# Kernel tuning notes

Hardware: AMD Instinct MI355X
Metric: run time of the kernel (lower is better)

Reference implementation:

```python
import jax, jax.numpy as jnp
import numpy as np

K = 3
STRIDE = 1
PADDING = 1
INVALID = -1.0


def _unfold(x, k, stride, padding, fill):
    # x: [B, C, H, W] -> patches [B, C, k, k, P] matching torch F.unfold ordering
    x = jnp.pad(x, ((0, 0), (0, 0), (padding, padding), (padding, padding)),
                constant_values=fill)
    # feature dim ordered channel-major (C, kh, kw), same as torch unfold
    p = jax.lax.conv_general_dilated_patches(x, (k, k), (stride, stride), 'VALID')
    b, _, ho, wo = p.shape
    c = x.shape[1]
    return p.reshape(b, c, k, k, ho * wo), ho, wo


def setup_inputs() -> dict:
    key = jax.random.key(0)
    k1, k2, k3, k4 = jax.random.split(key, 4)
    B, C, H, W = 8, 64, 128, 128
    OC = 64
    inp = jax.random.normal(k1, (B, C, H, W), dtype=jnp.float32)
    mask = jax.random.randint(k2, (B, H, W), 0, 4).astype(jnp.float32)
    conv = jax.random.normal(k3, (OC, C, K, K), dtype=jnp.float32) * 0.05
    bias = jax.random.normal(k4, (OC,), dtype=jnp.float32) * 0.05
    return {"inp": inp, "mask": mask, "conv": conv, "bias": bias}


def reference(inp, mask, conv, bias):
    k, stride, padding = K, STRIDE, PADDING
    b, c, h_in, w_in = inp.shape
    oc = conv.shape[0]
    center = (k - 1) // 2

    inp_patched, ho, wo = _unfold(inp, k, stride, padding, INVALID)       # [B,C,k,k,P]
    mask_patched, _, _ = _unfold(mask[:, None], k, stride, padding, INVALID)  # [B,1,k,k,P]
    mask_patched = mask_patched[:, 0]                                      # [B,k,k,P]

    center_val = mask_patched[:, center:center + 1, center:center + 1, :]  # [B,1,1,P]
    mask_eq = (mask_patched == center_val).astype(inp.dtype)               # [B,k,k,P]

    masked_input = inp_patched * mask_eq[:, None]                          # [B,C,k,k,P]
    m_norm = (k * k) / jnp.clip(mask_eq.reshape(b, k * k, -1).sum(axis=1), 1e-8)  # [B,P]

    masked_input = masked_input.reshape(b, c, k * k, -1)                   # [B,C,kk,P]
    w = conv.reshape(oc, c, k * k)                                         # [O,C,kk]
    out = jnp.einsum('bcxp,ocx->bop', masked_input, w)                     # [B,O,P]
    out = out * m_norm[:, None, :]
    out = out.reshape(b, oc, ho, wo)
    out = out + bias[None, :, None, None]

    mask_out = mask_patched[:, center, center, :].reshape(b, 1, ho, wo)
    return out, mask_out
```

## Files before the change

### kernel.cpp

```cpp
#include <hip/hip_runtime.h>
#include <stdint.h>

#define HW   128
#define CIN  64
#define OCN  64
#define NB   8

typedef __attribute__((ext_vector_type(8)))  short short8;
typedef __attribute__((ext_vector_type(16))) float floatx16;
typedef unsigned long long u64;

union F8 { short8 s; u64 u[2]; uint32_t d[4]; };

static __device__ __forceinline__ ushort f2bf(float f) {
    uint32_t u = __float_as_uint(f);
    uint32_t r = (u + 0x7FFFu + ((u >> 16) & 1u)) >> 16;
    return (ushort)r;
}

__global__ void wprep_kernel(const float* __restrict__ conv, ushort* __restrict__ wb) {
    int idx = blockIdx.x * 256 + threadIdx.x;
    int tap = idx >> 12;
    int r   = idx & 4095;
    int oc  = r >> 6;
    int c   = r & 63;
    wb[idx] = f2bf(conv[(oc * 64 + c) * 9 + tap]);
}

#define XS_CSTR 68
#define XS_ROW  (HW * XS_CSTR)
#define AS_STR  68
#define LDS_BYTES 80640

__global__ __launch_bounds__(256, 2)
void iconv_main(const float* __restrict__ inp, const float* __restrict__ mask,
                const ushort* __restrict__ wb, const float* __restrict__ bias,
                float* __restrict__ out)
{
    extern __shared__ char smem[];
    ushort* Xs = (ushort*)smem;
    ushort* As = Xs + 4 * XS_ROW;
    float*  Ms = (float*)(smem + 78336);
    float*  Bb = (float*)(smem + 78336 + 2048);

    const int tid  = threadIdx.x;
    const int bb   = blockIdx.x >> 6;
    const int y0   = (blockIdx.x & 63) << 1;
    const int lane = tid & 63;
    const int l31  = lane & 31;
    const int lh   = lane >> 5;
    const int w    = tid >> 6;
    const int yloc = w >> 1;
    const int xw   = (w & 1) * 64;
    const int y    = y0 + yloc;

    {
        const int cp = tid & 31;
        const int xq = (tid >> 5) * 16;
        const float* base0 = inp + ((size_t)(bb * CIN + 2 * cp) * HW) * HW;
        #pragma unroll
        for (int rr = 0; rr < 4; ++rr) {
            int gy = y0 - 1 + rr;
            if (gy >= 0 && gy < HW) {
                const float4* q0 = (const float4*)(base0 + (size_t)gy * HW + xq);
                const float4* q1 = (const float4*)(base0 + (size_t)HW * HW + (size_t)gy * HW + xq);
                float4 v0[4], v1[4];
                #pragma unroll
                for (int i = 0; i < 4; ++i) { v0[i] = q0[i]; v1[i] = q1[i]; }
                ushort* xrow = Xs + rr * XS_ROW + xq * XS_CSTR + 2 * cp;
                const float* f0 = (const float*)v0;
                const float* f1 = (const float*)v1;
                #pragma unroll
                for (int i = 0; i < 16; ++i) {
                    uint32_t p = (uint32_t)f2bf(f0[i]) | ((uint32_t)f2bf(f1[i]) << 16);
                    *(uint32_t*)(xrow + i * XS_CSTR) = p;
                }
            }
        }
    }
    {
        int rr = tid >> 6, x0 = (tid & 63) * 2;
        int gy = y0 - 1 + rr;
        if (gy >= 0 && gy < HW) {
            float2 v = *(const float2*)(mask + ((size_t)bb * HW + gy) * HW + x0);
            Ms[rr * HW + x0]     = v.x;
            Ms[rr * HW + x0 + 1] = v.y;
        }
    }
    if (tid < OCN) Bb[tid] = bias[tid];

    uint4 wv0 = *(const uint4*)(wb + tid * 16);
    uint4 wv1 = *(const uint4*)(wb + tid * 16 + 8);

    __syncthreads();

    uint32_t sel[9][2];
    float norm0, norm1;
    {
        int cnt0 = 0, cnt1 = 0;
        int xq0 = xw + l31, xq1 = xw + 32 + l31;
        float m00 = Ms[(1 + yloc) * HW + xq0];
        float m01 = Ms[(1 + yloc) * HW + xq1];
        #pragma unroll
        for (int t = 0; t < 9; ++t) {
            int dy = t / 3 - 1, dx = t % 3 - 1;
            int ny = y + dy;
            bool vy = (ny >= 0) && (ny < HW);
            int rbase = (1 + yloc + dy) * HW;
            {
                int nx = xq0 + dx;
                bool ok = vy && (nx >= 0) && (nx < HW);
                int nxc = nx < 0 ? 0 : (nx > HW - 1 ? HW - 1 : nx);
                bool eq = ok && (Ms[rbase + nxc] == m00);
                sel[t][0] = eq ? 0xFFFFFFFFu : 0u;
                cnt0 += eq ? 1 : 0;
            }
            {
                int nx = xq1 + dx;
                bool ok = vy && (nx >= 0) && (nx < HW);
                int nxc = nx < 0 ? 0 : (nx > HW - 1 ? HW - 1 : nx);
                bool eq = ok && (Ms[rbase + nxc] == m01);
                sel[t][1] = eq ? 0xFFFFFFFFu : 0u;
                cnt1 += eq ? 1 : 0;
            }
        }
        norm0 = 9.0f / (float)cnt0;
        norm1 = 9.0f / (float)cnt1;
    }

    floatx16 acc00 = {0,0,0,0,0,0,0,0,0,0,0,0,0,0,0,0};
    floatx16 acc01 = {0,0,0,0,0,0,0,0,0,0,0,0,0,0,0,0};
    floatx16 acc10 = {0,0,0,0,0,0,0,0,0,0,0,0,0,0,0,0};
    floatx16 acc11 = {0,0,0,0,0,0,0,0,0,0,0,0,0,0,0,0};

    const ushort* A0p = As + l31 * AS_STR + lh * 8;
    const ushort* A1p = As + (l31 + 32) * AS_STR + lh * 8;

    #pragma unroll
    for (int t = 0; t < 9; ++t) {
        if (t > 0) __syncthreads();
        {
            int oc = tid >> 2, c0 = (tid & 3) << 4;
            ushort* dst = As + oc * AS_STR + c0;
            *(uint2*)(dst)      = make_uint2(wv0.x, wv0.y);
            *(uint2*)(dst + 4)  = make_uint2(wv0.z, wv0.w);
            *(uint2*)(dst + 8)  = make_uint2(wv1.x, wv1.y);
            *(uint2*)(dst + 12) = make_uint2(wv1.z, wv1.w);
        }
        if (t < 8) {
            wv0 = *(const uint4*)(wb + (t + 1) * 4096 + tid * 16);
            wv1 = *(const uint4*)(wb + (t + 1) * 4096 + tid * 16 + 8);
        }
        __syncthreads();

        const int dy = t / 3 - 1, dx = t % 3 - 1;
        const int rrB = 1 + yloc + dy;
        int xa = xw + l31 + dx;
        int xb0c = xa < 0 ? 0 : (xa > HW - 1 ? HW - 1 : xa);
        int xa1 = xa + 32;
        int xb1c = xa1 < 0 ? 0 : (xa1 > HW - 1 ? HW - 1 : xa1);
        const ushort* B0p = Xs + rrB * XS_ROW + xb0c * XS_CSTR + lh * 8;
        const ushort* B1p = Xs + rrB * XS_ROW + xb1c * XS_CSTR + lh * 8;
        const uint32_t s0 = sel[t][0], s1 = sel[t][1];

        #pragma unroll
        for (int ks = 0; ks < 4; ++ks) {
            F8 a0, a1, b0, b1;
            a0.u[0] = *(const u64*)(A0p + ks * 16);
            a0.u[1] = *(const u64*)(A0p + ks * 16 + 4);
            a1.u[0] = *(const u64*)(A1p + ks * 16);
            a1.u[1] = *(const u64*)(A1p + ks * 16 + 4);
            b0.u[0] = *(const u64*)(B0p + ks * 16);
            b0.u[1] = *(const u64*)(B0p + ks * 16 + 4);
            b1.u[0] = *(const u64*)(B1p + ks * 16);
            b1.u[1] = *(const u64*)(B1p + ks * 16 + 4);
            b0.d[0] &= s0; b0.d[1] &= s0; b0.d[2] &= s0; b0.d[3] &= s0;
            b1.d[0] &= s1; b1.d[1] &= s1; b1.d[2] &= s1; b1.d[3] &= s1;
            acc00 = __builtin_amdgcn_mfma_f32_32x32x16_bf16(a0.s, b0.s, acc00, 0, 0, 0);
            acc01 = __builtin_amdgcn_mfma_f32_32x32x16_bf16(a0.s, b1.s, acc01, 0, 0, 0);
            acc10 = __builtin_amdgcn_mfma_f32_32x32x16_bf16(a1.s, b0.s, acc10, 0, 0, 0);
            acc11 = __builtin_amdgcn_mfma_f32_32x32x16_bf16(a1.s, b1.s, acc11, 0, 0, 0);
        }
    }

    float* outp = out + (size_t)bb * OCN * HW * HW + (size_t)y * HW;
    #pragma unroll
    for (int mt = 0; mt < 2; ++mt) {
        #pragma unroll
        for (int nt = 0; nt < 2; ++nt) {
            floatx16 a = (mt == 0) ? (nt == 0 ? acc00 : acc01)
                                   : (nt == 0 ? acc10 : acc11);
            float nm = (nt == 0) ? norm0 : norm1;
            int x = xw + nt * 32 + l31;
            #pragma unroll
            for (int r = 0; r < 16; ++r) {
                int oc = mt * 32 + (r & 3) + 8 * (r >> 2) + 4 * lh;
                outp[(size_t)oc * (HW * HW) + x] = a[r] * nm + Bb[oc];
            }
        }
    }
}

extern "C" void kernel_launch(void* const* d_in, const int* in_sizes, int n_in,
                              void* d_out, int out_size, void* d_ws, size_t ws_size,
                              hipStream_t stream) {
    (void)in_sizes; (void)n_in; (void)out_size; (void)ws_size;
    const float* inp  = (const float*)d_in[0];
    const float* mask = (const float*)d_in[1];
    const float* conv = (const float*)d_in[2];
    const float* bias = (const float*)d_in[3];
    float* out = (float*)d_out;
    ushort* wb = (ushort*)d_ws;

    hipFuncSetAttribute((const void*)iconv_main,
                        hipFuncAttributeMaxDynamicSharedMemorySize, LDS_BYTES);

    wprep_kernel<<<144, 256, 0, stream>>>(conv, wb);
    iconv_main<<<NB * (HW / 2), 256, LDS_BYTES, stream>>>(inp, mask, wb, bias, out);

    hipMemcpyAsync(out + (size_t)NB * OCN * HW * HW, mask,
                   (size_t)NB * HW * HW * sizeof(float),
                   hipMemcpyDeviceToDevice, stream);
}
```

Before: 104.9 us.

## Load MFMA-swizzled weights into registers, drop LDS weight staging and mask memcpy

The weight-prep kernel now writes weights already in MFMA A-operand lane order, so each wave loads its A fragments straight from global memory into registers and double-buffers them across taps. This removes the LDS weight tile and the two barriers per tap. The mask copy moves into the main kernel, replacing the separate device-to-device memcpy, and output stores become nontemporal. In exchange register pressure rises (16 uint4 of A fragments) and every wave fetches the weights redundantly from L2.

```diff
diff --git a/kernel.cpp b/kernel.cpp
--- a/kernel.cpp
+++ b/kernel.cpp
@@ -10,7 +10,7 @@
 typedef __attribute__((ext_vector_type(16))) float floatx16;
 typedef unsigned long long u64;
 
-union F8 { short8 s; u64 u[2]; uint32_t d[4]; };
+union F8 { short8 s; u64 u[2]; uint32_t d[4]; uint4 q; };
 
 static __device__ __forceinline__ ushort f2bf(float f) {
     uint32_t u = __float_as_uint(f);
@@ -19,18 +19,20 @@
 }
 
 __global__ void wprep_kernel(const float* __restrict__ conv, ushort* __restrict__ wb) {
-    int idx = blockIdx.x * 256 + threadIdx.x;
-    int tap = idx >> 12;
-    int r   = idx & 4095;
-    int oc  = r >> 6;
-    int c   = r & 63;
-    wb[idx] = f2bf(conv[(oc * 64 + c) * 9 + tap]);
+    int idx  = blockIdx.x * 256 + threadIdx.x;
+    int j    = idx & 7;
+    int lane = (idx >> 3) & 63;
+    int m    = (idx >> 9) & 1;
+    int ks   = (idx >> 10) & 3;
+    int t    = idx >> 12;
+    int oc   = m * 32 + (lane & 31);
+    int c    = ks * 16 + (lane >> 5) * 8 + j;
+    wb[idx] = f2bf(conv[(oc * 64 + c) * 9 + t]);
 }
 
 #define XS_CSTR 68
 #define XS_ROW  (HW * XS_CSTR)
-#define AS_STR  68
-#define LDS_BYTES 80640
+#define LDS_BYTES 71936
 
 __global__ __launch_bounds__(256, 2)
 void iconv_main(const float* __restrict__ inp, const float* __restrict__ mask,
@@ -39,9 +41,8 @@
 {
     extern __shared__ char smem[];
     ushort* Xs = (ushort*)smem;
-    ushort* As = Xs + 4 * XS_ROW;
-    float*  Ms = (float*)(smem + 78336);
-    float*  Bb = (float*)(smem + 78336 + 2048);
+    float*  Ms = (float*)(smem + 69632);
+    float*  Bb = (float*)(smem + 71680);
 
     const int tid  = threadIdx.x;
     const int bb   = blockIdx.x >> 6;
@@ -53,6 +54,12 @@
     const int yloc = w >> 1;
     const int xw   = (w & 1) * 64;
     const int y    = y0 + yloc;
+
+    const ushort* aBase = wb + lane * 8;
+    uint4 a_cur[8];
+    #pragma unroll
+    for (int f = 0; f < 8; ++f)
+        a_cur[f] = *(const uint4*)(aBase + f * 512);
 
     {
         const int cp = tid & 31;
@@ -89,10 +96,14 @@
     }
     if (tid < OCN) Bb[tid] = bias[tid];
 
-    uint4 wv0 = *(const uint4*)(wb + tid * 16);
-    uint4 wv1 = *(const uint4*)(wb + tid * 16 + 8);
-
     __syncthreads();
+
+    {
+        int yy = tid >> 7, x = tid & 127;
+        float mv = Ms[(1 + yy) * HW + x];
+        __builtin_nontemporal_store(
+            mv, out + (size_t)NB * OCN * HW * HW + ((size_t)bb * HW + y0 + yy) * HW + x);
+    }
 
     uint32_t sel[9][2];
     float norm0, norm1;
@@ -133,25 +144,14 @@
     floatx16 acc10 = {0,0,0,0,0,0,0,0,0,0,0,0,0,0,0,0};
     floatx16 acc11 = {0,0,0,0,0,0,0,0,0,0,0,0,0,0,0,0};
 
-    const ushort* A0p = As + l31 * AS_STR + lh * 8;
-    const ushort* A1p = As + (l31 + 32) * AS_STR + lh * 8;
-
     #pragma unroll
     for (int t = 0; t < 9; ++t) {
-        if (t > 0) __syncthreads();
-        {
-            int oc = tid >> 2, c0 = (tid & 3) << 4;
-            ushort* dst = As + oc * AS_STR + c0;
-            *(uint2*)(dst)      = make_uint2(wv0.x, wv0.y);
-            *(uint2*)(dst + 4)  = make_uint2(wv0.z, wv0.w);
-            *(uint2*)(dst + 8)  = make_uint2(wv1.x, wv1.y);
-            *(uint2*)(dst + 12) = make_uint2(wv1.z, wv1.w);
-        }
+        uint4 a_nxt[8];
         if (t < 8) {
-            wv0 = *(const uint4*)(wb + (t + 1) * 4096 + tid * 16);
-            wv1 = *(const uint4*)(wb + (t + 1) * 4096 + tid * 16 + 8);
-        }
-        __syncthreads();
+            #pragma unroll
+            for (int f = 0; f < 8; ++f)
+                a_nxt[f] = *(const uint4*)(aBase + ((t + 1) * 8 + f) * 512);
+        }
 
         const int dy = t / 3 - 1, dx = t % 3 - 1;
         const int rrB = 1 + yloc + dy;
@@ -166,10 +166,8 @@
         #pragma unroll
         for (int ks = 0; ks < 4; ++ks) {
             F8 a0, a1, b0, b1;
-            a0.u[0] = *(const u64*)(A0p + ks * 16);
-            a0.u[1] = *(const u64*)(A0p + ks * 16 + 4);
-            a1.u[0] = *(const u64*)(A1p + ks * 16);
-            a1.u[1] = *(const u64*)(A1p + ks * 16 + 4);
+            a0.q = a_cur[ks * 2 + 0];
+            a1.q = a_cur[ks * 2 + 1];
             b0.u[0] = *(const u64*)(B0p + ks * 16);
             b0.u[1] = *(const u64*)(B0p + ks * 16 + 4);
             b1.u[0] = *(const u64*)(B1p + ks * 16);
@@ -181,6 +179,10 @@
             acc10 = __builtin_amdgcn_mfma_f32_32x32x16_bf16(a1.s, b0.s, acc10, 0, 0, 0);
             acc11 = __builtin_amdgcn_mfma_f32_32x32x16_bf16(a1.s, b1.s, acc11, 0, 0, 0);
         }
+
+        #pragma unroll
+        for (int f = 0; f < 8; ++f)
+            if (t < 8) a_cur[f] = a_nxt[f];
     }
 
     float* outp = out + (size_t)bb * OCN * HW * HW + (size_t)y * HW;
@@ -195,7 +197,8 @@
             #pragma unroll
             for (int r = 0; r < 16; ++r) {
                 int oc = mt * 32 + (r & 3) + 8 * (r >> 2) + 4 * lh;
-                outp[(size_t)oc * (HW * HW) + x] = a[r] * nm + Bb[oc];
+                __builtin_nontemporal_store(a[r] * nm + Bb[oc],
+                                            outp + (size_t)oc * (HW * HW) + x);
             }
         }
     }
@@ -217,8 +220,4 @@
 
     wprep_kernel<<<144, 256, 0, stream>>>(conv, wb);
     iconv_main<<<NB * (HW / 2), 256, LDS_BYTES, stream>>>(inp, mask, wb, bias, out);
-
-    hipMemcpyAsync(out + (size_t)NB * OCN * HW * HW, mask,
-                   (size_t)NB * HW * HW * sizeof(float),
-                   hipMemcpyDeviceToDevice, stream);
-}
+}
```

New measurement: 103.6 us. Within noise of the previous version (-1.2%).
